# Kernel tuning notes

Hardware: AMD Instinct MI355X
Metric: run time of the kernel (lower is better)

The kernel has to match this reference:

```python
import jax, jax.numpy as jnp
import numpy as np
import math

B, C, D_FEAT, D_TASK, HID = 1024, 256, 512, 512, 32


def setup_inputs() -> dict:
    key = jax.random.key(0)
    ks = jax.random.split(key, 10)
    def xavier(k, shape, gain):
        fan_out, fan_in = shape
        a = gain * math.sqrt(6.0 / (fan_in + fan_out))
        return jax.random.uniform(k, shape, jnp.float32, -a, a)
    return {
        "Q": jax.random.normal(ks[0], (B, D_TASK), jnp.float32),
        "features": jax.random.normal(ks[1], (B, C, D_FEAT), jnp.float32),
        "Wk_w": xavier(ks[2], (D_TASK, D_FEAT), 0.1),
        "Wk_b": jnp.zeros((D_TASK,), jnp.float32),
        "Wv_w": xavier(ks[3], (D_TASK, D_FEAT), 0.1),
        "Wv_b": jnp.zeros((D_TASK,), jnp.float32),
        "g1_w": xavier(ks[4], (HID, D_TASK + 1), 1.0),
        "g1_b": jax.random.uniform(ks[5], (HID,), jnp.float32, -1.0, 1.0) / math.sqrt(D_TASK + 1),
        "g2_w": xavier(ks[6], (1, HID), 0.1),
        "g2_b": jnp.zeros((1,), jnp.float32),
    }


def reference(Q, features, Wk_w, Wk_b, Wv_w, Wv_b, g1_w, g1_b, g2_w, g2_b):
    # K, V projections: [B, C, d_task]
    K = jnp.einsum('bcf,tf->bct', features, Wk_w) + Wk_b
    V = jnp.einsum('bcf,tf->bct', features, Wv_w) + Wv_b
    # single-query cross-attention
    scores = jnp.einsum('bt,bct->bc', Q, K) / math.sqrt(D_TASK)  # [B, C]
    weights = jax.nn.softmax(scores, axis=-1)
    feat_read = jnp.einsum('bc,bct->bt', weights, V)  # [B, d_task]
    # gate from (Q, feature scale)
    feat_scale = jnp.mean(jnp.abs(features), axis=(1, 2), keepdims=False)[:, None]  # [B, 1]
    h = jnp.concatenate([Q, feat_scale], axis=-1)  # [B, d_task+1]
    h = jax.nn.gelu(h @ g1_w.T + g1_b, approximate=False)
    gate = jax.nn.sigmoid(h @ g2_w.T + g2_b)  # [B, 1]
    return gate * feat_read, gate
```

## Files before the change

### kernel.cpp

```cpp
#include <hip/hip_runtime.h>
#include <math.h>

constexpr int B = 1024, C = 256, DF = 512, DT = 512, HID = 32;

__global__ __launch_bounds__(256) void qproj_kernel(const float* __restrict__ Q,
                                                    const float* __restrict__ Wk,
                                                    float* __restrict__ qtil) {
    __shared__ __align__(16) float qs[4][DT];
    const int tid = threadIdx.x;
    const int b0 = blockIdx.x * 4;
#pragma unroll
    for (int bb = 0; bb < 4; bb++) {
        qs[bb][tid]       = Q[(b0 + bb) * DT + tid];
        qs[bb][tid + 256] = Q[(b0 + bb) * DT + tid + 256];
    }
    __syncthreads();
    const int f0 = tid * 2;
    float acc0[4] = {0.f, 0.f, 0.f, 0.f};
    float acc1[4] = {0.f, 0.f, 0.f, 0.f};
    for (int t4 = 0; t4 < DT; t4 += 4) {
        float q[4][4];
#pragma unroll
        for (int bb = 0; bb < 4; bb++) {
            float4 qv = *(const float4*)&qs[bb][t4];
            q[bb][0] = qv.x; q[bb][1] = qv.y; q[bb][2] = qv.z; q[bb][3] = qv.w;
        }
#pragma unroll
        for (int k = 0; k < 4; k++) {
            float2 w = *(const float2*)(Wk + (size_t)(t4 + k) * DF + f0);
#pragma unroll
            for (int bb = 0; bb < 4; bb++) {
                acc0[bb] += q[bb][k] * w.x;
                acc1[bb] += q[bb][k] * w.y;
            }
        }
    }
#pragma unroll
    for (int bb = 0; bb < 4; bb++) {
        float2 o; o.x = acc0[bb]; o.y = acc1[bb];
        *(float2*)(qtil + (size_t)(b0 + bb) * DF + f0) = o;
    }
}

__global__ __launch_bounds__(256) void main_kernel(
    const float* __restrict__ Q, const float* __restrict__ feat,
    const float* __restrict__ qtil,
    const float* __restrict__ Wv, const float* __restrict__ Wvb,
    const float* __restrict__ g1w, const float* __restrict__ g1b,
    const float* __restrict__ g2w, const float* __restrict__ g2b,
    float* __restrict__ out0, float* __restrict__ out1) {

    __shared__ __align__(16) float s_q[DF];
    __shared__ __align__(16) float s_Q[DT];
    __shared__ __align__(16) float s_part[4][DF];
    __shared__ __align__(16) float s_r[DF];
    __shared__ __align__(16) float s_out[DT];
    __shared__ float s_m[4], s_l[4], s_abs[4];
    __shared__ float s_hp[HID][8];
    __shared__ float s_h[HID];
    __shared__ float s_gate;

    const int tid  = threadIdx.x;
    const int lane = tid & 63;
    const int wv   = tid >> 6;
    const int b    = blockIdx.x;

    s_q[tid]       = qtil[b * DF + tid];
    s_q[tid + 256] = qtil[b * DF + tid + 256];
    s_Q[tid]       = Q[b * DT + tid];
    s_Q[tid + 256] = Q[b * DT + tid + 256];
    __syncthreads();

    float qreg[8];
    {
        float4 a0 = *(const float4*)&s_q[lane * 8];
        float4 a1 = *(const float4*)&s_q[lane * 8 + 4];
        qreg[0] = a0.x; qreg[1] = a0.y; qreg[2] = a0.z; qreg[3] = a0.w;
        qreg[4] = a1.x; qreg[5] = a1.y; qreg[6] = a1.z; qreg[7] = a1.w;
    }

    const float* fb = feat + (size_t)b * C * DF;
    float r[8] = {0.f, 0.f, 0.f, 0.f, 0.f, 0.f, 0.f, 0.f};
    float m = -INFINITY, l = 0.f, sabs = 0.f;
    const float rs = 0.044194173824159216f;

    for (int c = wv * 64; c < wv * 64 + 64; c += 2) {
        const float* row0 = fb + (size_t)c * DF + lane * 8;
        const float* row1 = row0 + DF;
        float4 x0a = *(const float4*)row0;
        float4 x0b = *(const float4*)(row0 + 4);
        float4 x1a = *(const float4*)row1;
        float4 x1b = *(const float4*)(row1 + 4);
        float v0[8] = {x0a.x, x0a.y, x0a.z, x0a.w, x0b.x, x0b.y, x0b.z, x0b.w};
        float v1[8] = {x1a.x, x1a.y, x1a.z, x1a.w, x1b.x, x1b.y, x1b.z, x1b.w};
        float dot0 = 0.f, dot1 = 0.f;
#pragma unroll
        for (int j = 0; j < 8; j++) {
            dot0 += v0[j] * qreg[j];
            dot1 += v1[j] * qreg[j];
            sabs += fabsf(v0[j]) + fabsf(v1[j]);
        }
#pragma unroll
        for (int off = 1; off < 64; off <<= 1) {
            dot0 += __shfl_xor(dot0, off, 64);
            dot1 += __shfl_xor(dot1, off, 64);
        }
        float s0 = dot0 * rs, s1 = dot1 * rs;
        float m2 = fmaxf(fmaxf(m, s0), s1);
        float a  = __expf(m - m2);
        float p0 = __expf(s0 - m2);
        float p1 = __expf(s1 - m2);
        l = l * a + p0 + p1;
#pragma unroll
        for (int j = 0; j < 8; j++) r[j] = r[j] * a + p0 * v0[j] + p1 * v1[j];
        m = m2;
    }
#pragma unroll
    for (int off = 1; off < 64; off <<= 1) sabs += __shfl_xor(sabs, off, 64);
    if (lane == 0) { s_m[wv] = m; s_l[wv] = l; s_abs[wv] = sabs; }
    __syncthreads();

    float M = fmaxf(fmaxf(s_m[0], s_m[1]), fmaxf(s_m[2], s_m[3]));
    float L = s_l[0] * __expf(s_m[0] - M) + s_l[1] * __expf(s_m[1] - M) +
              s_l[2] * __expf(s_m[2] - M) + s_l[3] * __expf(s_m[3] - M);
    float msc = __expf(m - M);
#pragma unroll
    for (int j = 0; j < 8; j++) s_part[wv][lane * 8 + j] = r[j] * msc;
    float fscale = (s_abs[0] + s_abs[1] + s_abs[2] + s_abs[3]) * (1.0f / (float)(C * DF));
    __syncthreads();

    float invL = 1.0f / L;
#pragma unroll
    for (int k = 0; k < 2; k++) {
        int f = tid + 256 * k;
        s_r[f] = (s_part[0][f] + s_part[1][f] + s_part[2][f] + s_part[3][f]) * invL;
    }

    {
        int i = tid >> 3, g = tid & 7;
        const float* row = g1w + (size_t)i * (DT + 1);
        float part = 0.f;
        for (int t = g * 64; t < g * 64 + 64; ++t) part += row[t] * s_Q[t];
        if (g == 0) part += row[DT] * fscale;
        s_hp[i][g] = part;
    }
    __syncthreads();
    if (tid < HID) {
        float x = g1b[tid];
#pragma unroll
        for (int g = 0; g < 8; ++g) x += s_hp[tid][g];
        s_h[tid] = 0.5f * x * (1.0f + erff(x * 0.70710678118654752f));
    }
    __syncthreads();
    if (tid == 0) {
        float z = g2b[0];
        for (int i = 0; i < HID; ++i) z += s_h[i] * g2w[i];
        float gate = 1.0f / (1.0f + __expf(-z));
        s_gate = gate;
        out1[b] = gate;
    }
    __syncthreads();

    float gate = s_gate;
    float rr[8];
    {
        float4 a0 = *(const float4*)&s_r[lane * 8];
        float4 a1 = *(const float4*)&s_r[lane * 8 + 4];
        rr[0] = a0.x; rr[1] = a0.y; rr[2] = a0.z; rr[3] = a0.w;
        rr[4] = a1.x; rr[5] = a1.y; rr[6] = a1.z; rr[7] = a1.w;
    }
    for (int t = wv * 128; t < wv * 128 + 128; t += 2) {
        const float* w0p = Wv + (size_t)t * DF + lane * 8;
        const float* w1p = w0p + DF;
        float4 w0a = *(const float4*)w0p;
        float4 w0b = *(const float4*)(w0p + 4);
        float4 w1a = *(const float4*)w1p;
        float4 w1b = *(const float4*)(w1p + 4);
        float dot0 = w0a.x * rr[0] + w0a.y * rr[1] + w0a.z * rr[2] + w0a.w * rr[3]
                   + w0b.x * rr[4] + w0b.y * rr[5] + w0b.z * rr[6] + w0b.w * rr[7];
        float dot1 = w1a.x * rr[0] + w1a.y * rr[1] + w1a.z * rr[2] + w1a.w * rr[3]
                   + w1b.x * rr[4] + w1b.y * rr[5] + w1b.z * rr[6] + w1b.w * rr[7];
#pragma unroll
        for (int off = 1; off < 64; off <<= 1) {
            dot0 += __shfl_xor(dot0, off, 64);
            dot1 += __shfl_xor(dot1, off, 64);
        }
        if (lane == 0) {
            s_out[t]     = gate * (dot0 + Wvb[t]);
            s_out[t + 1] = gate * (dot1 + Wvb[t + 1]);
        }
    }
    __syncthreads();
    float2 o;
    o.x = s_out[2 * tid];
    o.y = s_out[2 * tid + 1];
    *(float2*)(out0 + (size_t)b * DT + 2 * tid) = o;
}

extern "C" void kernel_launch(void* const* d_in, const int* in_sizes, int n_in,
                              void* d_out, int out_size, void* d_ws, size_t ws_size,
                              hipStream_t stream) {
    const float* Q    = (const float*)d_in[0];
    const float* feat = (const float*)d_in[1];
    const float* Wk   = (const float*)d_in[2];
    const float* Wv   = (const float*)d_in[4];
    const float* Wvb  = (const float*)d_in[5];
    const float* g1w  = (const float*)d_in[6];
    const float* g1b  = (const float*)d_in[7];
    const float* g2w  = (const float*)d_in[8];
    const float* g2b  = (const float*)d_in[9];
    float* out0 = (float*)d_out;
    float* out1 = out0 + (size_t)B * DT;
    float* qtil = (float*)d_ws;

    hipLaunchKernelGGL(qproj_kernel, dim3(B / 4), dim3(256), 0, stream, Q, Wk, qtil);
    hipLaunchKernelGGL(main_kernel, dim3(B), dim3(256), 0, stream,
                       Q, feat, qtil, Wv, Wvb, g1w, g1b, g2w, g2b, out0, out1);
}
```

Before: 793.0 us.

## Split feature streaming across two blocks per batch and batch the V readout

Splits the single fused kernel into a streaming kernel and a readout kernel. The streaming kernel uses two blocks per batch row, processes four rows per iteration and drops the online-max softmax rescaling, writing unnormalized partial sums to workspace. The readout kernel handles four batch rows per block and computes the Wv projection as a small batched GEMV against a pre-transposed Wv, so each weight load is reused across rows. The changes target low parallelism and the per-row rescaling and reduction overhead, at the cost of extra launches and workspace traffic. Skipping the max subtraction risks overflow if scores grow large.

```diff
diff --git a/kernel.cpp b/kernel.cpp
--- a/kernel.cpp
+++ b/kernel.cpp
@@ -2,6 +2,7 @@
 #include <math.h>
 
 constexpr int B = 1024, C = 256, DF = 512, DT = 512, HID = 32;
+
 
 __global__ __launch_bounds__(256) void qproj_kernel(const float* __restrict__ Q,
                                                     const float* __restrict__ Wk,
@@ -42,33 +43,34 @@
     }
 }
 
-__global__ __launch_bounds__(256) void main_kernel(
-    const float* __restrict__ Q, const float* __restrict__ feat,
-    const float* __restrict__ qtil,
-    const float* __restrict__ Wv, const float* __restrict__ Wvb,
-    const float* __restrict__ g1w, const float* __restrict__ g1b,
-    const float* __restrict__ g2w, const float* __restrict__ g2b,
-    float* __restrict__ out0, float* __restrict__ out1) {
-
+__global__ __launch_bounds__(256) void transpose_kernel(const float* __restrict__ Wv,
+                                                        float* __restrict__ WvT) {
+    __shared__ float tile[64][65];
+    const int bx = blockIdx.x & 7, by = blockIdx.x >> 3;
+    const int tx = threadIdx.x & 63, ty = threadIdx.x >> 6;
+#pragma unroll
+    for (int i = ty; i < 64; i += 4)
+        tile[i][tx] = Wv[(size_t)(64 * by + i) * DF + 64 * bx + tx];
+    __syncthreads();
+#pragma unroll
+    for (int i = ty; i < 64; i += 4)
+        WvT[(size_t)(64 * bx + i) * DT + 64 * by + tx] = tile[tx][i];
+}
+
+__global__ __launch_bounds__(256) void stream_kernel(
+    const float* __restrict__ feat, const float* __restrict__ qtil,
+    float* __restrict__ rpart, float* __restrict__ lpart, float* __restrict__ apart) {
     __shared__ __align__(16) float s_q[DF];
-    __shared__ __align__(16) float s_Q[DT];
     __shared__ __align__(16) float s_part[4][DF];
-    __shared__ __align__(16) float s_r[DF];
-    __shared__ __align__(16) float s_out[DT];
-    __shared__ float s_m[4], s_l[4], s_abs[4];
-    __shared__ float s_hp[HID][8];
-    __shared__ float s_h[HID];
-    __shared__ float s_gate;
-
+    __shared__ float s_l[4], s_abs[4];
     const int tid  = threadIdx.x;
     const int lane = tid & 63;
     const int wv   = tid >> 6;
-    const int b    = blockIdx.x;
+    const int b    = blockIdx.x >> 1;
+    const int half = blockIdx.x & 1;
 
     s_q[tid]       = qtil[b * DF + tid];
     s_q[tid + 256] = qtil[b * DF + tid + 256];
-    s_Q[tid]       = Q[b * DT + tid];
-    s_Q[tid + 256] = Q[b * DT + tid + 256];
     __syncthreads();
 
     float qreg[8];
@@ -79,122 +81,155 @@
         qreg[4] = a1.x; qreg[5] = a1.y; qreg[6] = a1.z; qreg[7] = a1.w;
     }
 
-    const float* fb = feat + (size_t)b * C * DF;
+    const float* fb = feat + ((size_t)b * C + half * (C / 2)) * DF;
     float r[8] = {0.f, 0.f, 0.f, 0.f, 0.f, 0.f, 0.f, 0.f};
-    float m = -INFINITY, l = 0.f, sabs = 0.f;
+    float l = 0.f, sabs = 0.f;
     const float rs = 0.044194173824159216f;
 
-    for (int c = wv * 64; c < wv * 64 + 64; c += 2) {
-        const float* row0 = fb + (size_t)c * DF + lane * 8;
-        const float* row1 = row0 + DF;
-        float4 x0a = *(const float4*)row0;
-        float4 x0b = *(const float4*)(row0 + 4);
-        float4 x1a = *(const float4*)row1;
-        float4 x1b = *(const float4*)(row1 + 4);
+    for (int c = wv * 32; c < wv * 32 + 32; c += 4) {
+        const float* row = fb + (size_t)c * DF + lane * 8;
+        float4 x0a = *(const float4*)(row);
+        float4 x0b = *(const float4*)(row + 4);
+        float4 x1a = *(const float4*)(row + DF);
+        float4 x1b = *(const float4*)(row + DF + 4);
+        float4 x2a = *(const float4*)(row + 2 * DF);
+        float4 x2b = *(const float4*)(row + 2 * DF + 4);
+        float4 x3a = *(const float4*)(row + 3 * DF);
+        float4 x3b = *(const float4*)(row + 3 * DF + 4);
         float v0[8] = {x0a.x, x0a.y, x0a.z, x0a.w, x0b.x, x0b.y, x0b.z, x0b.w};
         float v1[8] = {x1a.x, x1a.y, x1a.z, x1a.w, x1b.x, x1b.y, x1b.z, x1b.w};
-        float dot0 = 0.f, dot1 = 0.f;
+        float v2[8] = {x2a.x, x2a.y, x2a.z, x2a.w, x2b.x, x2b.y, x2b.z, x2b.w};
+        float v3[8] = {x3a.x, x3a.y, x3a.z, x3a.w, x3b.x, x3b.y, x3b.z, x3b.w};
+        float d0 = 0.f, d1 = 0.f, d2 = 0.f, d3 = 0.f;
 #pragma unroll
         for (int j = 0; j < 8; j++) {
-            dot0 += v0[j] * qreg[j];
-            dot1 += v1[j] * qreg[j];
-            sabs += fabsf(v0[j]) + fabsf(v1[j]);
+            d0 += v0[j] * qreg[j];
+            d1 += v1[j] * qreg[j];
+            d2 += v2[j] * qreg[j];
+            d3 += v3[j] * qreg[j];
+            sabs += fabsf(v0[j]) + fabsf(v1[j]) + fabsf(v2[j]) + fabsf(v3[j]);
         }
 #pragma unroll
         for (int off = 1; off < 64; off <<= 1) {
-            dot0 += __shfl_xor(dot0, off, 64);
-            dot1 += __shfl_xor(dot1, off, 64);
-        }
-        float s0 = dot0 * rs, s1 = dot1 * rs;
-        float m2 = fmaxf(fmaxf(m, s0), s1);
-        float a  = __expf(m - m2);
-        float p0 = __expf(s0 - m2);
-        float p1 = __expf(s1 - m2);
-        l = l * a + p0 + p1;
-#pragma unroll
-        for (int j = 0; j < 8; j++) r[j] = r[j] * a + p0 * v0[j] + p1 * v1[j];
-        m = m2;
+            d0 += __shfl_xor(d0, off, 64);
+            d1 += __shfl_xor(d1, off, 64);
+            d2 += __shfl_xor(d2, off, 64);
+            d3 += __shfl_xor(d3, off, 64);
+        }
+        float p0 = __expf(d0 * rs);
+        float p1 = __expf(d1 * rs);
+        float p2 = __expf(d2 * rs);
+        float p3 = __expf(d3 * rs);
+        l += p0 + p1 + p2 + p3;
+#pragma unroll
+        for (int j = 0; j < 8; j++)
+            r[j] += p0 * v0[j] + p1 * v1[j] + p2 * v2[j] + p3 * v3[j];
     }
 #pragma unroll
     for (int off = 1; off < 64; off <<= 1) sabs += __shfl_xor(sabs, off, 64);
-    if (lane == 0) { s_m[wv] = m; s_l[wv] = l; s_abs[wv] = sabs; }
-    __syncthreads();
-
-    float M = fmaxf(fmaxf(s_m[0], s_m[1]), fmaxf(s_m[2], s_m[3]));
-    float L = s_l[0] * __expf(s_m[0] - M) + s_l[1] * __expf(s_m[1] - M) +
-              s_l[2] * __expf(s_m[2] - M) + s_l[3] * __expf(s_m[3] - M);
-    float msc = __expf(m - M);
-#pragma unroll
-    for (int j = 0; j < 8; j++) s_part[wv][lane * 8 + j] = r[j] * msc;
-    float fscale = (s_abs[0] + s_abs[1] + s_abs[2] + s_abs[3]) * (1.0f / (float)(C * DF));
-    __syncthreads();
-
-    float invL = 1.0f / L;
+#pragma unroll
+    for (int j = 0; j < 8; j++) s_part[wv][lane * 8 + j] = r[j];
+    if (lane == 0) { s_l[wv] = l; s_abs[wv] = sabs; }
+    __syncthreads();
+
+    const size_t base = ((size_t)half * B + b) * DF;
 #pragma unroll
     for (int k = 0; k < 2; k++) {
         int f = tid + 256 * k;
-        s_r[f] = (s_part[0][f] + s_part[1][f] + s_part[2][f] + s_part[3][f]) * invL;
-    }
+        rpart[base + f] = s_part[0][f] + s_part[1][f] + s_part[2][f] + s_part[3][f];
+    }
+    if (tid == 0) {
+        lpart[half * B + b] = s_l[0] + s_l[1] + s_l[2] + s_l[3];
+        apart[half * B + b] = s_abs[0] + s_abs[1] + s_abs[2] + s_abs[3];
+    }
+}
+
+__global__ __launch_bounds__(256) void readout_kernel(
+    const float* __restrict__ Q, const float* __restrict__ WvT,
+    const float* __restrict__ Wvb,
+    const float* __restrict__ rpart, const float* __restrict__ lpart,
+    const float* __restrict__ apart,
+    const float* __restrict__ g1w, const float* __restrict__ g1b,
+    const float* __restrict__ g2w, const float* __restrict__ g2b,
+    float* __restrict__ out0, float* __restrict__ out1) {
+    __shared__ __align__(16) float s_r[4][DF];
+    __shared__ __align__(16) float s_Q[4][DT];
+    __shared__ float s_invL[4], s_fsc[4];
+    __shared__ float s_hp[4][HID][2];
+    __shared__ float s_h[4][HID];
+    __shared__ float s_gate[4];
+    const int tid = threadIdx.x;
+    const int b0 = blockIdx.x * 4;
+
+    if (tid < 4) {
+        float l = lpart[b0 + tid] + lpart[B + b0 + tid];
+        s_invL[tid] = 1.0f / l;
+        s_fsc[tid] = (apart[b0 + tid] + apart[B + b0 + tid]) * (1.0f / (float)(C * DF));
+    }
+#pragma unroll
+    for (int bb = 0; bb < 4; bb++) {
+#pragma unroll
+        for (int k = 0; k < 2; k++) {
+            int f = tid + 256 * k;
+            s_r[bb][f] = rpart[(size_t)(b0 + bb) * DF + f] +
+                         rpart[(size_t)(B + b0 + bb) * DF + f];
+            s_Q[bb][f] = Q[(size_t)(b0 + bb) * DT + f];
+        }
+    }
+    __syncthreads();
 
     {
-        int i = tid >> 3, g = tid & 7;
-        const float* row = g1w + (size_t)i * (DT + 1);
+        int bb = tid >> 6, i = (tid >> 1) & 31, g = tid & 1;
+        const float* row = g1w + (size_t)i * (DT + 1) + g * 256;
         float part = 0.f;
-        for (int t = g * 64; t < g * 64 + 64; ++t) part += row[t] * s_Q[t];
-        if (g == 0) part += row[DT] * fscale;
-        s_hp[i][g] = part;
-    }
-    __syncthreads();
-    if (tid < HID) {
-        float x = g1b[tid];
-#pragma unroll
-        for (int g = 0; g < 8; ++g) x += s_hp[tid][g];
-        s_h[tid] = 0.5f * x * (1.0f + erff(x * 0.70710678118654752f));
-    }
-    __syncthreads();
-    if (tid == 0) {
+        for (int t = 0; t < 256; ++t) part += row[t] * s_Q[bb][g * 256 + t];
+        if (g == 1) part += g1w[(size_t)i * (DT + 1) + DT] * s_fsc[bb];
+        s_hp[bb][i][g] = part;
+    }
+    __syncthreads();
+    if (tid < 128) {
+        int bb = tid >> 5, i = tid & 31;
+        float x = g1b[i] + s_hp[bb][i][0] + s_hp[bb][i][1];
+        s_h[bb][i] = 0.5f * x * (1.0f + erff(x * 0.70710678118654752f));
+    }
+    __syncthreads();
+    if (tid < 4) {
         float z = g2b[0];
-        for (int i = 0; i < HID; ++i) z += s_h[i] * g2w[i];
-        float gate = 1.0f / (1.0f + __expf(-z));
-        s_gate = gate;
-        out1[b] = gate;
-    }
-    __syncthreads();
-
-    float gate = s_gate;
-    float rr[8];
-    {
-        float4 a0 = *(const float4*)&s_r[lane * 8];
-        float4 a1 = *(const float4*)&s_r[lane * 8 + 4];
-        rr[0] = a0.x; rr[1] = a0.y; rr[2] = a0.z; rr[3] = a0.w;
-        rr[4] = a1.x; rr[5] = a1.y; rr[6] = a1.z; rr[7] = a1.w;
-    }
-    for (int t = wv * 128; t < wv * 128 + 128; t += 2) {
-        const float* w0p = Wv + (size_t)t * DF + lane * 8;
-        const float* w1p = w0p + DF;
-        float4 w0a = *(const float4*)w0p;
-        float4 w0b = *(const float4*)(w0p + 4);
-        float4 w1a = *(const float4*)w1p;
-        float4 w1b = *(const float4*)(w1p + 4);
-        float dot0 = w0a.x * rr[0] + w0a.y * rr[1] + w0a.z * rr[2] + w0a.w * rr[3]
-                   + w0b.x * rr[4] + w0b.y * rr[5] + w0b.z * rr[6] + w0b.w * rr[7];
-        float dot1 = w1a.x * rr[0] + w1a.y * rr[1] + w1a.z * rr[2] + w1a.w * rr[3]
-                   + w1b.x * rr[4] + w1b.y * rr[5] + w1b.z * rr[6] + w1b.w * rr[7];
-#pragma unroll
-        for (int off = 1; off < 64; off <<= 1) {
-            dot0 += __shfl_xor(dot0, off, 64);
-            dot1 += __shfl_xor(dot1, off, 64);
-        }
-        if (lane == 0) {
-            s_out[t]     = gate * (dot0 + Wvb[t]);
-            s_out[t + 1] = gate * (dot1 + Wvb[t + 1]);
-        }
-    }
-    __syncthreads();
-    float2 o;
-    o.x = s_out[2 * tid];
-    o.y = s_out[2 * tid + 1];
-    *(float2*)(out0 + (size_t)b * DT + 2 * tid) = o;
+        for (int i = 0; i < HID; ++i) z += s_h[tid][i] * g2w[i];
+        s_gate[tid] = 1.0f / (1.0f + __expf(-z));
+        out1[b0 + tid] = s_gate[tid];
+    }
+    __syncthreads();
+
+    const int t0 = tid * 2;
+    float acc0[4] = {0.f, 0.f, 0.f, 0.f};
+    float acc1[4] = {0.f, 0.f, 0.f, 0.f};
+    for (int f4 = 0; f4 < DF; f4 += 4) {
+        float rq[4][4];
+#pragma unroll
+        for (int bb = 0; bb < 4; bb++) {
+            float4 rv = *(const float4*)&s_r[bb][f4];
+            rq[bb][0] = rv.x; rq[bb][1] = rv.y; rq[bb][2] = rv.z; rq[bb][3] = rv.w;
+        }
+#pragma unroll
+        for (int k = 0; k < 4; k++) {
+            float2 w = *(const float2*)(WvT + (size_t)(f4 + k) * DT + t0);
+#pragma unroll
+            for (int bb = 0; bb < 4; bb++) {
+                acc0[bb] += rq[bb][k] * w.x;
+                acc1[bb] += rq[bb][k] * w.y;
+            }
+        }
+    }
+    float2 wb = *(const float2*)(Wvb + t0);
+#pragma unroll
+    for (int bb = 0; bb < 4; bb++) {
+        float g = s_gate[bb], il = s_invL[bb];
+        float2 o;
+        o.x = g * (il * acc0[bb] + wb.x);
+        o.y = g * (il * acc1[bb] + wb.y);
+        *(float2*)(out0 + (size_t)(b0 + bb) * DT + t0) = o;
+    }
 }
 
 extern "C" void kernel_launch(void* const* d_in, const int* in_sizes, int n_in,
@@ -211,9 +246,19 @@
     const float* g2b  = (const float*)d_in[9];
     float* out0 = (float*)d_out;
     float* out1 = out0 + (size_t)B * DT;
-    float* qtil = (float*)d_ws;
+
+    float* ws    = (float*)d_ws;
+    float* qtil  = ws;
+    float* WvT   = ws + 524288;
+    float* rpart = ws + 786432;
+    float* lpart = ws + 1835008;
+    float* apart = ws + 1837056;
 
     hipLaunchKernelGGL(qproj_kernel, dim3(B / 4), dim3(256), 0, stream, Q, Wk, qtil);
-    hipLaunchKernelGGL(main_kernel, dim3(B), dim3(256), 0, stream,
-                       Q, feat, qtil, Wv, Wvb, g1w, g1b, g2w, g2b, out0, out1);
-}
+    hipLaunchKernelGGL(transpose_kernel, dim3(64), dim3(256), 0, stream, Wv, WvT);
+    hipLaunchKernelGGL(stream_kernel, dim3(2 * B), dim3(256), 0, stream,
+                       feat, qtil, rpart, lpart, apart);
+    hipLaunchKernelGGL(readout_kernel, dim3(B / 4), dim3(256), 0, stream,
+                       Q, WvT, Wvb, rpart, lpart, apart,
+                       g1w, g1b, g2w, g2b, out0, out1);
+}
```

Measured after the change: 793.6 us. No clear change (+0.1%).
